# Performance work log

Measured on AMD Instinct MI355X. Metric: run time of the kernel, lower is better.

## Reference

```python
import jax, jax.numpy as jnp
import numpy as np
import math

E = 512
H = 2048
P = 128  # attention_limit

def _make_params(key):
    ks = jax.random.split(key, 6)
    s = 0.02
    p = {}
    p['wq'] = jax.random.normal(ks[0], (E, E), jnp.float32) * s
    p['bq'] = jnp.zeros((E,), jnp.float32)
    p['wk'] = jax.random.normal(ks[1], (E, E), jnp.float32) * s
    p['bk'] = jnp.zeros((E,), jnp.float32)
    p['wv'] = jax.random.normal(ks[2], (E, E), jnp.float32) * s
    p['bv'] = jnp.zeros((E,), jnp.float32)
    p['w1'] = jax.random.normal(ks[3], (E, H), jnp.float32) * s
    p['b1'] = jnp.zeros((H,), jnp.float32)
    p['w2'] = jax.random.normal(ks[4], (H, E), jnp.float32) * s
    p['b2'] = jnp.zeros((E,), jnp.float32)
    p['ln1_w'] = jnp.ones((E,), jnp.float32)
    p['ln1_b'] = jnp.zeros((E,), jnp.float32)
    p['ln2_w'] = jnp.ones((E,), jnp.float32)
    p['ln2_b'] = jnp.zeros((E,), jnp.float32)
    return p

def setup_inputs() -> dict:
    key = jax.random.key(0)
    kx, kp = jax.random.split(key)
    inp = {'x': jax.random.normal(kx, (2, 1024, E), jnp.float32)}
    inp.update(_make_params(kp))
    return inp

def _layernorm(x, w, b, eps=1e-5):
    mu = jnp.mean(x, axis=-1, keepdims=True)
    var = jnp.mean((x - mu) ** 2, axis=-1, keepdims=True)
    return (x - mu) / jnp.sqrt(var + eps) * w + b

def _forward(x, wq, bq, wk, bk, wv, bv, w1, b1, w2, b2, ln1_w, ln1_b, ln2_w, ln2_b):
    B, S, Ed = x.shape
    # "RoPE" is actually additive sinusoidal PE in the source
    pos = jnp.arange(S, dtype=jnp.float32)[:, None]
    div = jnp.exp(jnp.arange(0, Ed, 2, dtype=jnp.float32) * (-math.log(10000.0) / Ed))
    pe = jnp.zeros((S, Ed), jnp.float32)
    pe = pe.at[:, 0::2].set(jnp.sin(pos * div))
    pe = pe.at[:, 1::2].set(jnp.cos(pos * div))
    x = x + pe[None]

    # local attention: pad x first, then apply K/V linears (padded rows -> bias)
    x_ext = jnp.pad(x, ((0, 0), (P, P), (0, 0)))
    q = x @ wq + bq                      # [B,S,E]
    k_ext = x_ext @ wk + bk              # [B,S+2P,E]
    v_ext = x_ext @ wv + bv
    W = 2 * P + 1
    win_idx = jnp.arange(S)[:, None] + jnp.arange(W)[None, :]  # [S,W]
    k_win = k_ext[:, win_idx]            # [B,S,W,E]
    v_win = v_ext[:, win_idx]            # [B,S,W,E]
    energy = jnp.einsum('bse,bswe->bsw', q, k_win) / jnp.sqrt(jnp.float32(Ed))
    attn = jax.nn.softmax(energy, axis=-1)
    attn_out = jnp.einsum('bsw,bswe->bse', attn, v_win)

    x = _layernorm(attn_out + x, ln1_w, ln1_b)
    ff = jnp.maximum(x @ w1 + b1, 0.0) @ w2 + b2
    return _layernorm(ff + x, ln2_w, ln2_b)

def reference(x, wq, bq, wk, bk, wv, bv, w1, b1, w2, b2, ln1_w, ln1_b, ln2_w, ln2_b):
    return _forward(x, wq, bq, wk, bk, wv, bv, w1, b1, w2, b2, ln1_w, ln1_b, ln2_w, ln2_b)
```

## Files before the change

kernel.cpp:

```cpp
#include <hip/hip_runtime.h>
#include <hip/hip_bf16.h>

#define S_LEN 1024
#define E_DIM 512
#define H_DIM 2048
#define EXTA 1296
#define BS_ROWS 2048

typedef __attribute__((ext_vector_type(8))) short bf16x8;
typedef __attribute__((ext_vector_type(4))) float f32x4;

__device__ inline ushort f2bf(float x) {
  union { float f; unsigned u; } c; c.f = x;
  unsigned u = c.u;
  u += 0x7fffu + ((u >> 16) & 1u);
  return (ushort)(u >> 16);
}
__device__ inline float bf2f(ushort u) {
  union { unsigned u; float f; } c;
  c.u = ((unsigned)u) << 16;
  return c.f;
}

__device__ inline void gload16(ushort* dst, const ushort* src) {
  __builtin_amdgcn_global_load_lds(
      (const __attribute__((address_space(1))) void*)src,
      (__attribute__((address_space(3))) void*)dst, 16, 0, 0);
}

__global__ __launch_bounds__(256) void prep_kernel(const float* __restrict__ x,
                                                   const float* __restrict__ wq,
                                                   const float* __restrict__ wk,
                                                   const float* __restrict__ wv,
                                                   const float* __restrict__ bk,
                                                   const float* __restrict__ bv,
                                                   ushort* __restrict__ xpe_bf,
                                                   ushort* __restrict__ wqkvT,
                                                   ushort* __restrict__ k_bf,
                                                   ushort* __restrict__ v_t) {
  __shared__ float t[32][33];
  const int blk = blockIdx.x;
  if (blk < 1024) {
    int idx = blk * 256 + threadIdx.x;
    int ep = idx & 255;
    int s = idx >> 8;
    int e0 = ep * 2;
    const float c = -9.210340371976184f / 512.0f;
    float freq = __expf((float)e0 * c);
    float sn, cs;
    __sincosf((float)s * freq, &sn, &cs);
    size_t base = (size_t)s * E_DIM + e0;
    float2 x0 = *(const float2*)(x + base);
    float2 x1 = *(const float2*)(x + base + S_LEN * E_DIM);
    ushort2 o0, o1;
    o0.x = f2bf(x0.x + sn); o0.y = f2bf(x0.y + cs);
    o1.x = f2bf(x1.x + sn); o1.y = f2bf(x1.y + cs);
    *(ushort2*)(xpe_bf + base) = o0;
    *(ushort2*)(xpe_bf + base + S_LEN * E_DIM) = o1;
  } else if (blk < 1792) {
    const int tile = blk - 1024;
    const int sect = tile >> 8, tt = tile & 255;
    const float* W = sect == 0 ? wq : (sect == 1 ? wk : wv);
    ushort* WT = wqkvT + (size_t)sect * 512 * 512;
    const int bx = tt & 15, by = tt >> 4;
    int lx = threadIdx.x & 31, ly = threadIdx.x >> 5;
    int n0 = bx * 32, k0 = by * 32;
#pragma unroll
    for (int r = 0; r < 4; ++r)
      t[ly + r * 8][lx] = W[(size_t)(k0 + ly + r * 8) * 512 + n0 + lx];
    __syncthreads();
#pragma unroll
    for (int r = 0; r < 4; ++r)
      WT[(size_t)(n0 + ly + r * 8) * 512 + k0 + lx] = f2bf(t[lx][ly + r * 8]);
  } else {
    int p = (blk - 1792) * 256 + threadIdx.x;
    int t2 = p / (2 * 272 * 512);
    int r2 = p % (2 * 272 * 512);
    int b = r2 / (272 * 512);
    int r3 = r2 % (272 * 512);
    if (t2 == 0) {
      int rr = r3 >> 9, e = r3 & 511;
      int row = rr < 128 ? rr : 1024 + rr;
      float v = rr < 256 ? bk[e] : 0.f;
      k_bf[((size_t)b * EXTA + row) * 512 + e] = f2bf(v);
    } else {
      int n = r3 / 272, jj = r3 % 272;
      int j = jj < 128 ? jj : 1024 + jj;
      float v = jj < 256 ? bv[n] : 0.f;
      v_t[((size_t)b * 512 + n) * EXTA + j] = f2bf(v);
    }
  }
}

__global__ __launch_bounds__(256, 4) void qkv_kernel(const ushort* __restrict__ A,
                                                     const ushort* __restrict__ Bt,
                                                     const float* __restrict__ bq,
                                                     const float* __restrict__ bk,
                                                     const float* __restrict__ bv,
                                                     ushort* __restrict__ q_out,
                                                     ushort* __restrict__ k_out,
                                                     ushort* __restrict__ v_out) {
  __shared__ ushort As[2][64 * 64];
  __shared__ ushort Bs[2][64 * 64];
  const int blk = blockIdx.x;
  const int tid = threadIdx.x;
  const int lane = tid & 63;
  const int w = tid >> 6;
  const int wr = w >> 1, wc = w & 1;
  const int l15 = lane & 15, lhi = lane >> 4;
  const int col0 = (blk % 24) * 64, row0 = (blk / 24) * 64;

  int u0 = tid, u1 = 256 + tid;
  int ra0 = u0 >> 3, ca0 = ((u0 & 7) ^ (ra0 & 7)) * 8;
  int ra1 = u1 >> 3, ca1 = ((u1 & 7) ^ (ra1 & 7)) * 8;

  f32x4 acc[2][2] = {};

  gload16(&As[0][u0 * 8], &A[(size_t)(row0 + ra0) * 512 + ca0]);
  gload16(&As[0][u1 * 8], &A[(size_t)(row0 + ra1) * 512 + ca1]);
  gload16(&Bs[0][u0 * 8], &Bt[(size_t)(col0 + ra0) * 512 + ca0]);
  gload16(&Bs[0][u1 * 8], &Bt[(size_t)(col0 + ra1) * 512 + ca1]);

  for (int t = 0; t < 8; ++t) {
    const int cur = t & 1;
    if (t < 7) {
      int k0 = (t + 1) * 64;
      gload16(&As[cur ^ 1][u0 * 8], &A[(size_t)(row0 + ra0) * 512 + k0 + ca0]);
      gload16(&As[cur ^ 1][u1 * 8], &A[(size_t)(row0 + ra1) * 512 + k0 + ca1]);
      gload16(&Bs[cur ^ 1][u0 * 8], &Bt[(size_t)(col0 + ra0) * 512 + k0 + ca0]);
      gload16(&Bs[cur ^ 1][u1 * 8], &Bt[(size_t)(col0 + ra1) * 512 + k0 + ca1]);
      asm volatile("s_waitcnt vmcnt(4)" ::: "memory");
    } else {
      asm volatile("s_waitcnt vmcnt(0)" ::: "memory");
    }
    __builtin_amdgcn_s_barrier();
    __builtin_amdgcn_sched_barrier(0);
#pragma unroll
    for (int kk = 0; kk < 2; ++kk) {
      bf16x8 af[2], bfr[2];
#pragma unroll
      for (int mi = 0; mi < 2; ++mi) {
        int r = wr * 32 + mi * 16 + l15;
        int c16 = (kk * 4 + lhi) ^ (r & 7);
        af[mi] = *(const bf16x8*)&As[cur][r * 64 + c16 * 8];
      }
#pragma unroll
      for (int ni = 0; ni < 2; ++ni) {
        int r = wc * 32 + ni * 16 + l15;
        int c16 = (kk * 4 + lhi) ^ (r & 7);
        bfr[ni] = *(const bf16x8*)&Bs[cur][r * 64 + c16 * 8];
      }
#pragma unroll
      for (int mi = 0; mi < 2; ++mi)
#pragma unroll
        for (int ni = 0; ni < 2; ++ni)
          acc[mi][ni] = __builtin_amdgcn_mfma_f32_16x16x32_bf16(af[mi], bfr[ni], acc[mi][ni], 0, 0, 0);
    }
    __builtin_amdgcn_sched_barrier(0);
    __builtin_amdgcn_s_barrier();
  }

#pragma unroll
  for (int mi = 0; mi < 2; ++mi) {
    int mbase = row0 + wr * 32 + mi * 16 + lhi * 4;
#pragma unroll
    for (int ni = 0; ni < 2; ++ni) {
      int n = col0 + wc * 32 + ni * 16 + l15;
      int sect = n >> 9, nn = n & 511;
      float b = sect == 0 ? bq[nn] : (sect == 1 ? bk[nn] : bv[nn]);
      int bb = mbase >> 10;
      int s = mbase & 1023;
      if (sect == 0) {
#pragma unroll
        for (int j = 0; j < 4; ++j)
          q_out[(size_t)(mbase + j) * 512 + nn] = f2bf(acc[mi][ni][j] + b);
      } else if (sect == 1) {
#pragma unroll
        for (int j = 0; j < 4; ++j)
          k_out[((size_t)bb * EXTA + 128 + s + j) * 512 + nn] = f2bf(acc[mi][ni][j] + b);
      } else {
        ushort4 pk;
        pk.x = f2bf(acc[mi][ni][0] + b);
        pk.y = f2bf(acc[mi][ni][1] + b);
        pk.z = f2bf(acc[mi][ni][2] + b);
        pk.w = f2bf(acc[mi][ni][3] + b);
        *(ushort4*)&v_out[((size_t)bb * 512 + nn) * EXTA + 128 + s] = pk;
      }
    }
  }
}

template <int OUT>
__global__ __launch_bounds__(256, 4) void mfma_gemm(const ushort* __restrict__ A,
                                                    const ushort* __restrict__ Bt,
                                                    const float* __restrict__ bias,
                                                    void* __restrict__ Cout,
                                                    int M, int N, int K, int LDA) {
  __shared__ ushort As[2][64 * 64];
  __shared__ ushort Bs[2][64 * 64];
  const int tid = threadIdx.x;
  const int lane = tid & 63;
  const int w = tid >> 6;
  const int wr = w >> 1, wc = w & 1;
  const int l15 = lane & 15, lhi = lane >> 4;
  const int col0 = blockIdx.x * 64, row0 = blockIdx.y * 64;
  const int koff = blockIdx.z * K;
  const int nt = K >> 6;

  int u0 = tid, u1 = 256 + tid;
  int ra0 = u0 >> 3, ca0 = ((u0 & 7) ^ (ra0 & 7)) * 8;
  int ra1 = u1 >> 3, ca1 = ((u1 & 7) ^ (ra1 & 7)) * 8;
  const ushort* Abase = A + (size_t)row0 * LDA + koff;
  const ushort* Bbase = Bt + (size_t)col0 * LDA + koff;

  f32x4 acc[2][2] = {};

  gload16(&As[0][u0 * 8], &Abase[(size_t)ra0 * LDA + ca0]);
  gload16(&As[0][u1 * 8], &Abase[(size_t)ra1 * LDA + ca1]);
  gload16(&Bs[0][u0 * 8], &Bbase[(size_t)ra0 * LDA + ca0]);
  gload16(&Bs[0][u1 * 8], &Bbase[(size_t)ra1 * LDA + ca1]);

  for (int t = 0; t < nt; ++t) {
    const int cur = t & 1;
    if (t + 1 < nt) {
      int k0 = (t + 1) * 64;
      gload16(&As[cur ^ 1][u0 * 8], &Abase[(size_t)ra0 * LDA + k0 + ca0]);
      gload16(&As[cur ^ 1][u1 * 8], &Abase[(size_t)ra1 * LDA + k0 + ca1]);
      gload16(&Bs[cur ^ 1][u0 * 8], &Bbase[(size_t)ra0 * LDA + k0 + ca0]);
      gload16(&Bs[cur ^ 1][u1 * 8], &Bbase[(size_t)ra1 * LDA + k0 + ca1]);
      asm volatile("s_waitcnt vmcnt(4)" ::: "memory");
    } else {
      asm volatile("s_waitcnt vmcnt(0)" ::: "memory");
    }
    __builtin_amdgcn_s_barrier();
    __builtin_amdgcn_sched_barrier(0);
#pragma unroll
    for (int kk = 0; kk < 2; ++kk) {
      bf16x8 af[2], bfr[2];
#pragma unroll
      for (int mi = 0; mi < 2; ++mi) {
        int r = wr * 32 + mi * 16 + l15;
        int c16 = (kk * 4 + lhi) ^ (r & 7);
        af[mi] = *(const bf16x8*)&As[cur][r * 64 + c16 * 8];
      }
#pragma unroll
      for (int ni = 0; ni < 2; ++ni) {
        int r = wc * 32 + ni * 16 + l15;
        int c16 = (kk * 4 + lhi) ^ (r & 7);
        bfr[ni] = *(const bf16x8*)&Bs[cur][r * 64 + c16 * 8];
      }
#pragma unroll
      for (int mi = 0; mi < 2; ++mi)
#pragma unroll
        for (int ni = 0; ni < 2; ++ni)
          acc[mi][ni] = __builtin_amdgcn_mfma_f32_16x16x32_bf16(af[mi], bfr[ni], acc[mi][ni], 0, 0, 0);
    }
    __builtin_amdgcn_sched_barrier(0);
    __builtin_amdgcn_s_barrier();
  }

#pragma unroll
  for (int mi = 0; mi < 2; ++mi) {
    int mbase = row0 + wr * 32 + mi * 16 + lhi * 4;
#pragma unroll
    for (int ni = 0; ni < 2; ++ni) {
      int n = col0 + wc * 32 + ni * 16 + l15;
      if constexpr (OUT == 1) {
        float b = bias[n];
        ushort* C = (ushort*)Cout;
#pragma unroll
        for (int j = 0; j < 4; ++j)
          C[(size_t)(mbase + j) * N + n] = f2bf(fmaxf(acc[mi][ni][j] + b, 0.f));
      } else {
        float* C = (float*)Cout + (size_t)blockIdx.z * M * N;
#pragma unroll
        for (int j = 0; j < 4; ++j) C[(size_t)(mbase + j) * N + n] = acc[mi][ni][j];
      }
    }
  }
}

union AttnSm {
  struct {
    float e[16][292];
    ushort p[16][296];
    float inv[16];
    float redS[16][16];
    float redQ[16][16];
    float mu[16], rs[16];
  } a;
  float t[32][33];
};

__global__ __launch_bounds__(1024) void attn_ln1(const ushort* __restrict__ qb,
                                                 const ushort* __restrict__ kb,
                                                 const ushort* __restrict__ vt,
                                                 const ushort* __restrict__ xpe_bf,
                                                 const float* __restrict__ ln1w,
                                                 const float* __restrict__ ln1b,
                                                 const float* __restrict__ w1,
                                                 const float* __restrict__ w2,
                                                 ushort* __restrict__ w1T,
                                                 ushort* __restrict__ w2T,
                                                 ushort* __restrict__ x1bf) {
  __shared__ AttnSm sm;
  const int tid = threadIdx.x;

  if (blockIdx.x >= 128) {
    const int tile = blockIdx.x - 128;
    const float* W; ushort* WT; int K, N, bx, by;
    if (tile < 1024) {
      K = 512; N = 2048; W = w1; WT = w1T;
      bx = tile & 63; by = tile >> 6;
    } else {
      K = 2048; N = 512; W = w2; WT = w2T;
      int tt = tile - 1024; bx = tt & 15; by = tt >> 4;
    }
    int lx = tid & 31, ly = tid >> 5;
    int n0 = bx * 32, k0 = by * 32;
    sm.t[ly][lx] = W[(size_t)(k0 + ly) * N + n0 + lx];
    __syncthreads();
    WT[(size_t)(n0 + ly) * K + k0 + lx] = f2bf(sm.t[lx][ly]);
    return;
  }

  const int lane = tid & 63;
  const int w = tid >> 6;
  const int l15 = lane & 15, lhi = lane >> 4;
  const int tile = blockIdx.x;
  const int b = tile >> 6;
  const int s0 = (tile & 63) * 16;
  const int base0 = b * 1024 + s0;

  const ushort* qrow = qb + (size_t)(base0 + l15) * 512 + lhi * 8;
  bf16x8 qf[16];
#pragma unroll
  for (int ks = 0; ks < 16; ++ks) qf[ks] = *(const bf16x8*)(qrow + ks * 32);

  const float scale = 0.044194173824159216f;
  const ushort* kbase = kb + (size_t)b * EXTA * 512 + (size_t)(s0 + l15) * 512 + lhi * 8;

  for (int jt = w; jt < 18; jt += 16) {
    f32x4 acc = {};
    const ushort* kp = kbase + (size_t)jt * 16 * 512;
#pragma unroll
    for (int ks = 0; ks < 16; ++ks) {
      bf16x8 kf = *(const bf16x8*)(kp + ks * 32);
      acc = __builtin_amdgcn_mfma_f32_16x16x32_bf16(qf[ks], kf, acc, 0, 0, 0);
    }
    int jc = jt * 16 + l15;
#pragma unroll
    for (int j = 0; j < 4; ++j) {
      int i = lhi * 4 + j;
      bool valid = (jc >= i) && (jc <= i + 256);
      sm.a.e[i][jc] = valid ? acc[j] * scale : -1e30f;
    }
  }
  __syncthreads();

  {
    int r = w;
    float m = -1e30f;
#pragma unroll
    for (int t = 0; t < 5; ++t) {
      int col = lane + 64 * t;
      float e = (t < 4 || lane < 32) ? sm.a.e[r][col] : -1e30f;
      m = fmaxf(m, e);
    }
#pragma unroll
    for (int off = 1; off <= 32; off <<= 1) m = fmaxf(m, __shfl_xor(m, off));
    float s = 0.f;
#pragma unroll
    for (int t = 0; t < 5; ++t) {
      int col = lane + 64 * t;
      if (t < 4 || lane < 32) {
        float p = __expf(sm.a.e[r][col] - m);
        s += p;
        sm.a.p[r][col] = f2bf(p);
      }
    }
#pragma unroll
    for (int off = 1; off <= 32; off <<= 1) s += __shfl_xor(s, off);
    if (lane == 0) sm.a.inv[r] = 1.0f / s;
  }
  __syncthreads();

  bf16x8 pf[9];
#pragma unroll
  for (int ks = 0; ks < 9; ++ks) pf[ks] = *(const bf16x8*)&sm.a.p[l15][ks * 32 + lhi * 8];
  float inv[4];
#pragma unroll
  for (int j = 0; j < 4; ++j) inv[j] = sm.a.inv[lhi * 4 + j];

  const ushort* vbase = vt + (size_t)b * 512 * EXTA + s0 + lhi * 8;
  float val[2][4];
#pragma unroll
  for (int ni = 0; ni < 2; ++ni) {
    int n = w * 32 + ni * 16 + l15;
    f32x4 acc = {};
    const ushort* vp = vbase + (size_t)n * EXTA;
#pragma unroll
    for (int ks = 0; ks < 9; ++ks) {
      bf16x8 vf = *(const bf16x8*)(vp + ks * 32);
      acc = __builtin_amdgcn_mfma_f32_16x16x32_bf16(pf[ks], vf, acc, 0, 0, 0);
    }
#pragma unroll
    for (int j = 0; j < 4; ++j) {
      int r = lhi * 4 + j;
      val[ni][j] = acc[j] * inv[j] + bf2f(xpe_bf[(size_t)(base0 + r) * 512 + n]);
    }
  }

  float S[4], Q[4];
#pragma unroll
  for (int j = 0; j < 4; ++j) {
    S[j] = 0.f; Q[j] = 0.f;
#pragma unroll
    for (int ni = 0; ni < 2; ++ni) { S[j] += val[ni][j]; Q[j] += val[ni][j] * val[ni][j]; }
  }
#pragma unroll
  for (int off = 1; off <= 8; off <<= 1) {
#pragma unroll
    for (int j = 0; j < 4; ++j) {
      S[j] += __shfl_xor(S[j], off);
      Q[j] += __shfl_xor(Q[j], off);
    }
  }
  if (l15 == 0) {
#pragma unroll
    for (int j = 0; j < 4; ++j) { sm.a.redS[w][lhi * 4 + j] = S[j]; sm.a.redQ[w][lhi * 4 + j] = Q[j]; }
  }
  __syncthreads();
  if (tid < 16) {
    float sS = 0.f, sQ = 0.f;
#pragma unroll
    for (int ww = 0; ww < 16; ++ww) { sS += sm.a.redS[ww][tid]; sQ += sm.a.redQ[ww][tid]; }
    float mu = sS * (1.0f / 512.0f);
    float var = sQ * (1.0f / 512.0f) - mu * mu;
    sm.a.mu[tid] = mu;
    sm.a.rs[tid] = rsqrtf(var + 1e-5f);
  }
  __syncthreads();

#pragma unroll
  for (int ni = 0; ni < 2; ++ni) {
    int n = w * 32 + ni * 16 + l15;
    float lw = ln1w[n], lb = ln1b[n];
#pragma unroll
    for (int j = 0; j < 4; ++j) {
      int r = lhi * 4 + j;
      float o = (val[ni][j] - sm.a.mu[r]) * sm.a.rs[r] * lw + lb;
      x1bf[(size_t)(base0 + r) * 512 + n] = f2bf(o);
    }
  }
}

__device__ inline float wave_reduce_sum(float v) {
#pragma unroll
  for (int off = 32; off >= 1; off >>= 1) v += __shfl_xor(v, off);
  return v;
}

__global__ __launch_bounds__(256) void ln2_kernel(const float* __restrict__ parts,
                                                  const float* __restrict__ ab,
                                                  const ushort* __restrict__ rsd_bf,
                                                  const float* __restrict__ w,
                                                  const float* __restrict__ bias,
                                                  float* __restrict__ out) {
  const int row = blockIdx.x;
  const int tid = threadIdx.x;
  __shared__ float red[8];
  const int e0 = tid * 2;
  const size_t base = (size_t)row * E_DIM + e0;
  const size_t PART = (size_t)BS_ROWS * E_DIM;
  float2 v0 = *(const float2*)(parts + base);
  float2 v1 = *(const float2*)(parts + PART + base);
  float2 bb = *(const float2*)(ab + e0);
  ushort2 rv = *(const ushort2*)(rsd_bf + base);
  float x0 = v0.x + v1.x + bb.x + bf2f(rv.x);
  float x1 = v0.y + v1.y + bb.y + bf2f(rv.y);

  float sm = wave_reduce_sum(x0 + x1);
  if ((tid & 63) == 0) red[tid >> 6] = sm;
  __syncthreads();
  float mu = (red[0] + red[1] + red[2] + red[3]) * (1.0f / 512.0f);
  float d0 = x0 - mu, d1 = x1 - mu;
  float vs = wave_reduce_sum(d0 * d0 + d1 * d1);
  if ((tid & 63) == 0) red[4 + (tid >> 6)] = vs;
  __syncthreads();
  float var = (red[4] + red[5] + red[6] + red[7]) * (1.0f / 512.0f);
  float inv = rsqrtf(var + 1e-5f);
  float2 wv = *(const float2*)(w + e0);
  float2 bi = *(const float2*)(bias + e0);
  float o0 = d0 * inv * wv.x + bi.x;
  float o1 = d1 * inv * wv.y + bi.y;
  *(float2*)(out + base) = make_float2(o0, o1);
}

extern "C" void kernel_launch(void* const* d_in, const int* in_sizes, int n_in,
                              void* d_out, int out_size, void* d_ws, size_t ws_size,
                              hipStream_t stream) {
  const float* x    = (const float*)d_in[0];
  const float* wq   = (const float*)d_in[1];
  const float* bq   = (const float*)d_in[2];
  const float* wk   = (const float*)d_in[3];
  const float* bk   = (const float*)d_in[4];
  const float* wv   = (const float*)d_in[5];
  const float* bv   = (const float*)d_in[6];
  const float* w1   = (const float*)d_in[7];
  const float* b1   = (const float*)d_in[8];
  const float* w2   = (const float*)d_in[9];
  const float* b2   = (const float*)d_in[10];
  const float* ln1w = (const float*)d_in[11];
  const float* ln1b = (const float*)d_in[12];
  const float* ln2w = (const float*)d_in[13];
  const float* ln2b = (const float*)d_in[14];

  char* W = (char*)d_ws;
  ushort* xpebf  = (ushort*)(W);
  ushort* wqkvT  = (ushort*)(W + (2u  << 20));
  ushort* w1T    = (ushort*)(W + (4u  << 20));
  ushort* w2T    = (ushort*)(W + (6u  << 20));
  ushort* q_bf   = (ushort*)(W + (8u  << 20));
  ushort* k_bf   = (ushort*)(W + (10u << 20));
  ushort* v_t    = (ushort*)(W + (13u << 20));
  ushort* x1bf   = (ushort*)(W + (16u << 20));
  ushort* ff1_bf = (ushort*)(W + (18u << 20));
  float*  ff2    = (float*)(W + (26u << 20));

  prep_kernel<<<3968, 256, 0, stream>>>(x, wq, wk, wv, bk, bv,
                                        xpebf, wqkvT, k_bf, v_t);

  qkv_kernel<<<768, 256, 0, stream>>>(xpebf, wqkvT, bq, bk, bv, q_bf, k_bf, v_t);

  attn_ln1<<<2176, 1024, 0, stream>>>(q_bf, k_bf, v_t, xpebf, ln1w, ln1b,
                                      w1, w2, w1T, w2T, x1bf);

  mfma_gemm<1><<<dim3(32, 32), 256, 0, stream>>>(
      x1bf, w1T, b1, ff1_bf, BS_ROWS, H_DIM, 512, 512);

  mfma_gemm<3><<<dim3(8, 32, 2), 256, 0, stream>>>(
      ff1_bf, w2T, nullptr, ff2, BS_ROWS, E_DIM, 1024, 2048);

  ln2_kernel<<<BS_ROWS, 256, 0, stream>>>(ff2, b2, x1bf, ln2w, ln2b, (float*)d_out);
}
```

Measured before the change: 71.37 us.

## Swizzle block IDs for XCD locality and drop split-K in second FFN GEMM

Block indices in the QKV, attention and FFN GEMM kernels are remapped so that consecutive tiles land on the same XCD (blockIdx & 7 groups), aiming to improve L2 reuse of shared A/B panels across the MI355X's chiplets. The second FFN GEMM stops splitting K into two partial outputs; each block now runs the full K=2048, and ln2 reads one partial buffer instead of summing two. This removes a partial-sum write and read, but halves the block count of that GEMM to 256, which lowers parallelism and lengthens each block's serial K loop.

```diff
diff --git a/kernel.cpp b/kernel.cpp
--- a/kernel.cpp
+++ b/kernel.cpp
@@ -102,7 +102,7 @@
                                                      ushort* __restrict__ v_out) {
   __shared__ ushort As[2][64 * 64];
   __shared__ ushort Bs[2][64 * 64];
-  const int blk = blockIdx.x;
+  const int blk = (blockIdx.x & 7) * 96 + (blockIdx.x >> 3);
   const int tid = threadIdx.x;
   const int lane = tid & 63;
   const int w = tid >> 6;
@@ -190,7 +190,7 @@
   }
 }
 
-template <int OUT>
+template <int OUT, int CHUNK, int NCOL>
 __global__ __launch_bounds__(256, 4) void mfma_gemm(const ushort* __restrict__ A,
                                                     const ushort* __restrict__ Bt,
                                                     const float* __restrict__ bias,
@@ -198,20 +198,20 @@
                                                     int M, int N, int K, int LDA) {
   __shared__ ushort As[2][64 * 64];
   __shared__ ushort Bs[2][64 * 64];
+  const int blk = (blockIdx.x & 7) * CHUNK + (blockIdx.x >> 3);
   const int tid = threadIdx.x;
   const int lane = tid & 63;
   const int w = tid >> 6;
   const int wr = w >> 1, wc = w & 1;
   const int l15 = lane & 15, lhi = lane >> 4;
-  const int col0 = blockIdx.x * 64, row0 = blockIdx.y * 64;
-  const int koff = blockIdx.z * K;
+  const int col0 = (blk % NCOL) * 64, row0 = (blk / NCOL) * 64;
   const int nt = K >> 6;
 
   int u0 = tid, u1 = 256 + tid;
   int ra0 = u0 >> 3, ca0 = ((u0 & 7) ^ (ra0 & 7)) * 8;
   int ra1 = u1 >> 3, ca1 = ((u1 & 7) ^ (ra1 & 7)) * 8;
-  const ushort* Abase = A + (size_t)row0 * LDA + koff;
-  const ushort* Bbase = Bt + (size_t)col0 * LDA + koff;
+  const ushort* Abase = A + (size_t)row0 * LDA;
+  const ushort* Bbase = Bt + (size_t)col0 * LDA;
 
   f32x4 acc[2][2] = {};
 
@@ -272,7 +272,7 @@
         for (int j = 0; j < 4; ++j)
           C[(size_t)(mbase + j) * N + n] = f2bf(fmaxf(acc[mi][ni][j] + b, 0.f));
       } else {
-        float* C = (float*)Cout + (size_t)blockIdx.z * M * N;
+        float* C = (float*)Cout;
 #pragma unroll
         for (int j = 0; j < 4; ++j) C[(size_t)(mbase + j) * N + n] = acc[mi][ni][j];
       }
@@ -327,7 +327,7 @@
   const int lane = tid & 63;
   const int w = tid >> 6;
   const int l15 = lane & 15, lhi = lane >> 4;
-  const int tile = blockIdx.x;
+  const int tile = (blockIdx.x & 7) * 16 + (blockIdx.x >> 3);
   const int b = tile >> 6;
   const int s0 = (tile & 63) * 16;
   const int base0 = b * 1024 + s0;
@@ -461,7 +461,7 @@
   return v;
 }
 
-__global__ __launch_bounds__(256) void ln2_kernel(const float* __restrict__ parts,
+__global__ __launch_bounds__(256) void ln2_kernel(const float* __restrict__ ff2,
                                                   const float* __restrict__ ab,
                                                   const ushort* __restrict__ rsd_bf,
                                                   const float* __restrict__ w,
@@ -472,13 +472,11 @@
   __shared__ float red[8];
   const int e0 = tid * 2;
   const size_t base = (size_t)row * E_DIM + e0;
-  const size_t PART = (size_t)BS_ROWS * E_DIM;
-  float2 v0 = *(const float2*)(parts + base);
-  float2 v1 = *(const float2*)(parts + PART + base);
+  float2 v0 = *(const float2*)(ff2 + base);
   float2 bb = *(const float2*)(ab + e0);
   ushort2 rv = *(const ushort2*)(rsd_bf + base);
-  float x0 = v0.x + v1.x + bb.x + bf2f(rv.x);
-  float x1 = v0.y + v1.y + bb.y + bf2f(rv.y);
+  float x0 = v0.x + bb.x + bf2f(rv.x);
+  float x1 = v0.y + bb.y + bf2f(rv.y);
 
   float sm = wave_reduce_sum(x0 + x1);
   if ((tid & 63) == 0) red[tid >> 6] = sm;
@@ -536,11 +534,11 @@
   attn_ln1<<<2176, 1024, 0, stream>>>(q_bf, k_bf, v_t, xpebf, ln1w, ln1b,
                                       w1, w2, w1T, w2T, x1bf);
 
-  mfma_gemm<1><<<dim3(32, 32), 256, 0, stream>>>(
+  mfma_gemm<1, 128, 32><<<1024, 256, 0, stream>>>(
       x1bf, w1T, b1, ff1_bf, BS_ROWS, H_DIM, 512, 512);
 
-  mfma_gemm<3><<<dim3(8, 32, 2), 256, 0, stream>>>(
-      ff1_bf, w2T, nullptr, ff2, BS_ROWS, E_DIM, 1024, 2048);
+  mfma_gemm<0, 32, 8><<<256, 256, 0, stream>>>(
+      ff1_bf, w2T, nullptr, ff2, BS_ROWS, E_DIM, 2048, 2048);
 
   ln2_kernel<<<BS_ROWS, 256, 0, stream>>>(ff2, b2, x1bf, ln2w, ln2b, (float*)d_out);
 }
```

After: 77.91 us. +9.2%, slower.
